# Kernel optimization log

Measured on AMD Instinct MI355X. Metric: run time of the kernel, lower is better.

Reference implementation:

```python
import jax, jax.numpy as jnp
import numpy as np

D_MODEL, D_STATE, D_CONV, EXPAND = 1024, 16, 4, 2
D_INNER = EXPAND * D_MODEL           # 2048
DT_RANK = D_MODEL // 16              # 64
BATCH, SEQLEN = 2, 2048


def setup_inputs() -> dict:
    key = jax.random.key(0)
    ks = jax.random.split(key, 10)
    s = 0.02
    hidden_states = jax.random.normal(ks[0], (BATCH, SEQLEN, D_MODEL), jnp.float32)
    in_proj_w = jax.random.normal(ks[1], (2 * D_INNER, D_MODEL), jnp.float32) * s
    conv_w = jax.random.normal(ks[2], (D_INNER, 1, D_CONV), jnp.float32) * 0.3
    conv_b = jax.random.normal(ks[3], (D_INNER,), jnp.float32) * 0.1
    x_proj_w = jax.random.normal(ks[4], (DT_RANK + 2 * D_STATE, D_INNER), jnp.float32) * s
    dt_init_std = DT_RANK ** -0.5
    dt_proj_w = jax.random.uniform(ks[5], (D_INNER, DT_RANK), jnp.float32,
                                   minval=-dt_init_std, maxval=dt_init_std)
    # bias = inverse-softplus of dt sampled log-uniform in [1e-3, 1e-1]
    dt = jnp.exp(jax.random.uniform(ks[6], (D_INNER,), jnp.float32)
                 * (np.log(0.1) - np.log(0.001)) + np.log(0.001))
    dt = jnp.clip(dt, 1e-4, None)
    dt_proj_b = dt + jnp.log(-jnp.expm1(-dt))
    # A = repeat(arange(1, d_state+1), 'n -> d n')
    A_log = jnp.log(jnp.tile(jnp.arange(1, D_STATE + 1, dtype=jnp.float32), (D_INNER, 1)))
    Dp = jnp.ones((D_INNER,), jnp.float32)
    out_proj_w = jax.random.normal(ks[7], (D_MODEL, D_INNER), jnp.float32) * s
    return {
        'hidden_states': hidden_states, 'in_proj_w': in_proj_w,
        'conv_w': conv_w, 'conv_b': conv_b, 'x_proj_w': x_proj_w,
        'dt_proj_w': dt_proj_w, 'dt_proj_b': dt_proj_b,
        'A_log': A_log, 'D': Dp, 'out_proj_w': out_proj_w,
    }


def _mamba_fwd(hidden_states, in_proj_w, conv_w, conv_b, x_proj_w,
               dt_proj_w, dt_proj_b, A_log, D, out_proj_w):
    d_inner = in_proj_w.shape[0] // 2
    d_conv = conv_w.shape[-1]
    dt_rank = dt_proj_w.shape[1]
    d_state = A_log.shape[1]
    b = hidden_states.shape[0]

    # in_proj then split into x / z gate branches  -> [B, L, d_inner] each
    xz = hidden_states @ in_proj_w.T
    x, z = jnp.split(xz, 2, axis=-1)

    # depthwise causal conv1d + SiLU (pad left d_conv-1 == padding=d_conv-1 then trim)
    xc = x.transpose(0, 2, 1)                       # [B, d_inner, L]
    xc = jax.lax.conv_general_dilated(
        xc, conv_w, window_strides=(1,), padding=[(d_conv - 1, 0)],
        dimension_numbers=('NCH', 'OIH', 'NCH'), feature_group_count=d_inner)
    xl = jax.nn.silu(xc + conv_b[None, :, None]).transpose(0, 2, 1)  # [B, L, d_inner]

    # x_proj -> dt, B, C
    x_dbl = xl @ x_proj_w.T                         # [B, L, dt_rank + 2*d_state]
    dt, Bm, Cm = jnp.split(x_dbl, [dt_rank, dt_rank + d_state], axis=-1)
    delta = jax.nn.softplus(dt @ dt_proj_w.T + dt_proj_b)  # [B, L, d_inner]

    A = -jnp.exp(A_log)                             # [d_inner, d_state]

    def step(h, inputs):
        u_t, d_t, b_t, c_t = inputs  # [B,d_inner], [B,d_inner], [B,d_state], [B,d_state]
        dA = jnp.exp(d_t[..., None] * A)                      # [B, d_inner, d_state]
        h = dA * h + (d_t * u_t)[..., None] * b_t[:, None, :]
        y_t = jnp.einsum('bdn,bn->bd', h, c_t)
        return h, y_t

    h0 = jnp.zeros((b, d_inner, d_state), hidden_states.dtype)
    xs = (xl.transpose(1, 0, 2), delta.transpose(1, 0, 2),
          Bm.transpose(1, 0, 2), Cm.transpose(1, 0, 2))
    _, ys = jax.lax.scan(step, h0, xs)              # ys: [L, B, d_inner]
    y = ys.transpose(1, 0, 2)

    y = y + xl * D                                  # skip (D) term
    y = y * jax.nn.silu(z)                          # gate
    return y @ out_proj_w.T                         # [B, L, d_model]


def reference(hidden_states, in_proj_w, conv_w, conv_b, x_proj_w,
              dt_proj_w, dt_proj_b, A_log, D, out_proj_w):
    return _mamba_fwd(hidden_states, in_proj_w, conv_w, conv_b, x_proj_w,
                      dt_proj_w, dt_proj_b, A_log, D, out_proj_w)
```

## Files before the change

kernel.cpp:

```cpp
#include <hip/hip_runtime.h>

#define D_MODEL 1024
#define D_STATE 16
#define D_CONV  4
#define D_INNER 2048
#define DT_RANK 64
#define BATCH   2
#define SEQLEN  2048
#define NTOK    (BATCH * SEQLEN)
#define NCH     64
#define LC      (SEQLEN / NCH)
#define XKS     8
#define XNC     96


__device__ __forceinline__ float bf2f(unsigned short v) {
    union { unsigned int u; float f; } c; c.u = ((unsigned int)v) << 16; return c.f;
}
__device__ __forceinline__ unsigned short f2bf(float f) {
    union { unsigned int u; float f; } c; c.f = f;
    unsigned int r = c.u + 0x7FFF + ((c.u >> 16) & 1);
    return (unsigned short)(r >> 16);
}

__device__ __forceinline__ int sniff_bf(const void* Dp) {
    return (((const unsigned int*)Dp)[0] == 0x3F803F80u) ? 1 : 0;
}

__device__ __forceinline__ float ldF(const void* p, size_t idx, int isbf) {
    return isbf ? bf2f(((const unsigned short*)p)[idx]) : ((const float*)p)[idx];
}
__device__ __forceinline__ void ld16f(const float* p, float* o) {
#pragma unroll
    for (int q = 0; q < 4; q++) {
        float4 v = *(const float4*)(p + 4 * q);
        o[4 * q + 0] = v.x; o[4 * q + 1] = v.y; o[4 * q + 2] = v.z; o[4 * q + 3] = v.w;
    }
}

#define CVT_N0 (NTOK * D_MODEL)
#define CVT_N1 (2 * D_INNER * D_MODEL)
#define CVT_N2 (D_MODEL * D_INNER)
#define CVT_N3 (D_INNER * DT_RANK)
#define CVT_TOT (CVT_N0 + CVT_N1 + CVT_N2 + CVT_N3)

__device__ __forceinline__ void cvt8(const void* in, unsigned short* out,
                                     size_t e0, int isbf)
{
    if (isbf) {
        *(uint4*)(out + e0) = *(const uint4*)((const unsigned short*)in + e0);
    } else {
        const float* f = (const float*)in + e0;
        float4 a = *(const float4*)f;
        float4 b = *(const float4*)(f + 4);
        ushort4 o0 = { f2bf(a.x), f2bf(a.y), f2bf(a.z), f2bf(a.w) };
        ushort4 o1 = { f2bf(b.x), f2bf(b.y), f2bf(b.z), f2bf(b.w) };
        *(ushort4*)(out + e0)     = o0;
        *(ushort4*)(out + e0 + 4) = o1;
    }
}

__launch_bounds__(256)
__global__ void cvt_all(const void* __restrict__ hid, const void* __restrict__ ipw,
                        const void* __restrict__ opw, const void* __restrict__ dtw,
                        unsigned short* __restrict__ hidB, unsigned short* __restrict__ ipwB,
                        unsigned short* __restrict__ opwB, unsigned short* __restrict__ dtwB,
                        const void* __restrict__ Dp)
{
    const int isbf = sniff_bf(Dp);
    size_t e = ((size_t)blockIdx.x * 256 + threadIdx.x) * 8;
    if (e < CVT_N0) { cvt8(hid, hidB, e, isbf); return; }
    e -= CVT_N0;
    if (e < CVT_N1) { cvt8(ipw, ipwB, e, isbf); return; }
    e -= CVT_N1;
    if (e < CVT_N2) { cvt8(opw, opwB, e, isbf); return; }
    e -= CVT_N2;
    if (e < CVT_N3) { cvt8(dtw, dtwB, e, isbf); }
}

typedef __attribute__((ext_vector_type(8))) __bf16 bf16x8;
typedef __attribute__((ext_vector_type(4))) float  f32x4;

__global__ void mfma_probe(int* __restrict__ dmap) {
    __shared__ alignas(16) unsigned short As[16 * 32];
    __shared__ alignas(16) unsigned short Bs[16 * 32];
    const int t = threadIdx.x;
    const int q = t >> 4, l15 = t & 15;

    for (int idx = t; idx < 512; idx += 64) {
        As[idx] = f2bf((float)(idx >> 5));
        Bs[idx] = f2bf(0.03125f);
    }
    __syncthreads();
    bf16x8 a1 = *(const bf16x8*)&As[l15 * 32 + q * 8];
    bf16x8 b1 = *(const bf16x8*)&Bs[l15 * 32 + q * 8];
    f32x4 acc1 = {0.f, 0.f, 0.f, 0.f};
    acc1 = __builtin_amdgcn_mfma_f32_16x16x32_bf16(a1, b1, acc1, 0, 0, 0);
    __syncthreads();

    for (int idx = t; idx < 512; idx += 64) {
        As[idx] = f2bf(0.03125f);
        Bs[idx] = f2bf((float)(idx >> 5));
    }
    __syncthreads();
    bf16x8 a2 = *(const bf16x8*)&As[l15 * 32 + q * 8];
    bf16x8 b2 = *(const bf16x8*)&Bs[l15 * 32 + q * 8];
    f32x4 acc2 = {0.f, 0.f, 0.f, 0.f};
    acc2 = __builtin_amdgcn_mfma_f32_16x16x32_bf16(a2, b2, acc2, 0, 0, 0);

#pragma unroll
    for (int r = 0; r < 4; r++) {
        int ma = (int)(acc1[r] + 0.5f);
        int nb = (int)(acc2[r] + 0.5f);
        if (ma < 0 || ma > 15 || nb < 0 || nb > 15) { ma = q * 4 + r; nb = l15; }
        dmap[t * 4 + r] = ma | (nb << 4);
    }
}

__device__ __forceinline__ void gl2lds16(const void* g, void* l) {
    __builtin_amdgcn_global_load_lds(
        (const __attribute__((address_space(1))) unsigned int*)g,
        (__attribute__((address_space(3))) unsigned int*)l,
        16, 0, 0);
}

__device__ __forceinline__ void stage_half(const unsigned short* __restrict__ G,
                                           int grow0, int K, int k0,
                                           unsigned short* ldsAB, int half, int t)
{
    const int r8  = t >> 3;
    const int c8  = t & 7;
    const int swz = (c8 ^ (r8 & 7)) << 3;
#pragma unroll
    for (int j = 0; j < 2; j++) {
        const int row = half * 128 + j * 64 + r8;
        gl2lds16(&G[(size_t)(grow0 + row) * K + k0 + swz],
                 &ldsAB[row * 64 + c8 * 8]);
    }
}

__device__ __forceinline__ bf16x8 ldsfrag(const unsigned short* p, int row, int slot) {
    return *(const bf16x8*)&p[row * 64 + ((slot ^ (row & 7)) << 3)];
}

__launch_bounds__(512)
__global__ void gemm1_8ph(const unsigned short* __restrict__ A,
                          const unsigned short* __restrict__ B,
                          float* __restrict__ C,
                          int M, int N, int K,
                          const int* __restrict__ dmap)
{
    extern __shared__ __align__(16) unsigned short lds[];
    unsigned short* A0l = lds;
    unsigned short* B0l = lds + 16384;
    unsigned short* A1l = lds + 32768;
    unsigned short* B1l = lds + 49152;

    const int t    = threadIdx.x;
    const int lane = t & 63;
    const int w    = t >> 6;
    const int wm   = (w >> 2) * 128, wn = (w & 3) * 64;
    const int q    = lane >> 4, l15 = lane & 15;

    const int nbn  = N >> 8;
    const int nwg  = (M >> 8) * nbn;
    const int orig = blockIdx.x;
    const int wg   = (orig & 7) * (nwg >> 3) + (orig >> 3);
    const int bm   = wg / nbn, bn = wg % nbn;
    const int m0   = bm << 8, n0 = bn << 8;
    const int NT   = K >> 6;

    int mp[4];
#pragma unroll
    for (int r = 0; r < 4; r++) mp[r] = dmap[lane * 4 + r];

    f32x4 acc[8][4];
#pragma unroll
    for (int i = 0; i < 8; i++)
#pragma unroll
        for (int j = 0; j < 4; j++) acc[i][j] = (f32x4){0.f, 0.f, 0.f, 0.f};

    stage_half(B, n0, K, 0, B0l, 0, t);
    stage_half(B, n0, K, 0, B0l, 1, t);
    stage_half(A, m0, K, 0, A0l, 0, t);
    stage_half(A, m0, K, 0, A0l, 1, t);
    {
        const int k1 = (NT > 1 ? 64 : 0);
        stage_half(B, n0, K, k1, B1l, 0, t);
        stage_half(B, n0, K, k1, B1l, 1, t);
    }
    asm volatile("s_waitcnt vmcnt(4)" ::: "memory");
    __builtin_amdgcn_s_barrier();

#pragma unroll 2
    for (int tt = 0; tt < NT; ++tt) {
        const int p = tt & 1;
        const unsigned short* Ac = p ? A1l : A0l;
        const unsigned short* Bc = p ? B1l : B0l;
        unsigned short* Anx = p ? A0l : A1l;
        unsigned short* Bnx = p ? B1l : B0l;
        const int kA = (tt + 1 < NT ? tt + 1 : 0) << 6;
        const int kB = (tt + 2 < NT ? tt + 2 : 0) << 6;

        bf16x8 af[4][2], b0r[2][2], b1r[2][2];

#pragma unroll
        for (int i = 0; i < 4; i++)
#pragma unroll
            for (int ks = 0; ks < 2; ks++)
                af[i][ks] = ldsfrag(Ac, wm + i * 16 + l15, ks * 4 + q);
#pragma unroll
        for (int j = 0; j < 2; j++)
#pragma unroll
            for (int ks = 0; ks < 2; ks++)
                b0r[j][ks] = ldsfrag(Bc, wn + j * 16 + l15, ks * 4 + q);
        stage_half(A, m0, K, kA, Anx, 0, t);
        asm volatile("" ::: "memory");
        __builtin_amdgcn_s_barrier();
        __builtin_amdgcn_s_setprio(1);
#pragma unroll
        for (int i = 0; i < 4; i++)
#pragma unroll
            for (int j = 0; j < 2; j++)
#pragma unroll
                for (int ks = 0; ks < 2; ks++)
                    acc[i][j] = __builtin_amdgcn_mfma_f32_16x16x32_bf16(
                        af[i][ks], b0r[j][ks], acc[i][j], 0, 0, 0);
        __builtin_amdgcn_s_setprio(0);
        asm volatile("" ::: "memory");
        __builtin_amdgcn_s_barrier();

#pragma unroll
        for (int j = 0; j < 2; j++)
#pragma unroll
            for (int ks = 0; ks < 2; ks++)
                b1r[j][ks] = ldsfrag(Bc, wn + 32 + j * 16 + l15, ks * 4 + q);
        stage_half(A, m0, K, kA, Anx, 1, t);
        asm volatile("" ::: "memory");
        __builtin_amdgcn_s_barrier();
        __builtin_amdgcn_s_setprio(1);
#pragma unroll
        for (int i = 0; i < 4; i++)
#pragma unroll
            for (int j = 0; j < 2; j++)
#pragma unroll
                for (int ks = 0; ks < 2; ks++)
                    acc[i][2 + j] = __builtin_amdgcn_mfma_f32_16x16x32_bf16(
                        af[i][ks], b1r[j][ks], acc[i][2 + j], 0, 0, 0);
        __builtin_amdgcn_s_setprio(0);
        asm volatile("" ::: "memory");
        __builtin_amdgcn_s_barrier();

#pragma unroll
        for (int i = 0; i < 4; i++)
#pragma unroll
            for (int ks = 0; ks < 2; ks++)
                af[i][ks] = ldsfrag(Ac, wm + 64 + i * 16 + l15, ks * 4 + q);
        stage_half(B, n0, K, kB, Bnx, 0, t);
        asm volatile("" ::: "memory");
        __builtin_amdgcn_s_barrier();
        __builtin_amdgcn_s_setprio(1);
#pragma unroll
        for (int i = 0; i < 4; i++)
#pragma unroll
            for (int j = 0; j < 2; j++)
#pragma unroll
                for (int ks = 0; ks < 2; ks++)
                    acc[4 + i][2 + j] = __builtin_amdgcn_mfma_f32_16x16x32_bf16(
                        af[i][ks], b1r[j][ks], acc[4 + i][2 + j], 0, 0, 0);
        __builtin_amdgcn_s_setprio(0);
        asm volatile("" ::: "memory");
        __builtin_amdgcn_s_barrier();

        stage_half(B, n0, K, kB, Bnx, 1, t);
        asm volatile("" ::: "memory");
        __builtin_amdgcn_s_barrier();
        __builtin_amdgcn_s_setprio(1);
#pragma unroll
        for (int i = 0; i < 4; i++)
#pragma unroll
            for (int j = 0; j < 2; j++)
#pragma unroll
                for (int ks = 0; ks < 2; ks++)
                    acc[4 + i][j] = __builtin_amdgcn_mfma_f32_16x16x32_bf16(
                        af[i][ks], b0r[j][ks], acc[4 + i][j], 0, 0, 0);
        __builtin_amdgcn_s_setprio(0);
        asm volatile("s_waitcnt vmcnt(4)" ::: "memory");
        __builtin_amdgcn_s_barrier();
    }

#pragma unroll
    for (int i = 0; i < 8; i++) {
#pragma unroll
        for (int r = 0; r < 4; r++) {
            const int mo = mp[r] & 15, no = mp[r] >> 4;
            const int m = m0 + wm + i * 16 + mo;
#pragma unroll
            for (int j = 0; j < 4; j++) {
                const int n = n0 + wn + j * 16 + no;
                C[(size_t)m * N + n] = acc[i][j][r];
            }
        }
    }
}

__device__ __forceinline__ void stage_op(const unsigned short* __restrict__ A,
                                         const unsigned short* __restrict__ B,
                                         int m0, int n0, int K, int k0,
                                         unsigned short* Al, unsigned short* Bl, int t)
{
    const int r   = t >> 3;
    const int c8  = t & 7;
    const int swz = (c8 ^ (r & 7)) << 3;
#pragma unroll
    for (int j = 0; j < 4; j++) {
        const int row = j * 32 + r;
        gl2lds16(&A[(size_t)(m0 + row) * K + k0 + swz], &Al[row * 64 + c8 * 8]);
    }
#pragma unroll
    for (int j = 0; j < 2; j++) {
        const int row = j * 32 + r;
        gl2lds16(&B[(size_t)(n0 + row) * K + k0 + swz], &Bl[row * 64 + c8 * 8]);
    }
}

__launch_bounds__(256)
__global__ void gemm_op_2ph(const unsigned short* __restrict__ A,
                            const unsigned short* __restrict__ B,
                            float* __restrict__ C,
                            const int* __restrict__ dmap)
{
    constexpr int M = NTOK, N = D_MODEL, K = D_INNER;
    constexpr int NT = K / 64;
    __shared__ alignas(16) unsigned short Al[2][128 * 64];
    __shared__ alignas(16) unsigned short Bl[2][64 * 64];

    const int t    = threadIdx.x;
    const int lane = t & 63;
    const int w    = t >> 6;
    const int wm   = (w >> 1) * 64, wn = (w & 1) * 32;
    const int q    = lane >> 4, l15 = lane & 15;

    const int nbn  = N / 64;
    const int nwg  = (M / 128) * nbn;
    const int orig = blockIdx.x;
    const int wg   = (orig & 7) * (nwg >> 3) + (orig >> 3);
    const int bm   = wg / nbn, bn = wg % nbn;
    const int m0   = bm * 128, n0 = bn * 64;

    int mp[4];
#pragma unroll
    for (int r = 0; r < 4; r++) mp[r] = dmap[lane * 4 + r];

    f32x4 acc[4][2];
#pragma unroll
    for (int i = 0; i < 4; i++)
#pragma unroll
        for (int j = 0; j < 2; j++) acc[i][j] = (f32x4){0.f, 0.f, 0.f, 0.f};

    stage_op(A, B, m0, n0, K, 0, Al[0], Bl[0], t);
    asm volatile("s_waitcnt vmcnt(0)" ::: "memory");
    __builtin_amdgcn_s_barrier();

#pragma unroll 2
    for (int tt = 0; tt < NT - 1; ++tt) {
        const int cur = tt & 1;
        stage_op(A, B, m0, n0, K, (tt + 1) * 64, Al[cur ^ 1], Bl[cur ^ 1], t);

        bf16x8 af[4][2], bfr[2][2];
#pragma unroll
        for (int i = 0; i < 4; i++)
#pragma unroll
            for (int ks = 0; ks < 2; ks++)
                af[i][ks] = ldsfrag(Al[cur], wm + i * 16 + l15, ks * 4 + q);
#pragma unroll
        for (int j = 0; j < 2; j++)
#pragma unroll
            for (int ks = 0; ks < 2; ks++)
                bfr[j][ks] = ldsfrag(Bl[cur], wn + j * 16 + l15, ks * 4 + q);
        __builtin_amdgcn_s_setprio(1);
#pragma unroll
        for (int i = 0; i < 4; i++)
#pragma unroll
            for (int j = 0; j < 2; j++)
#pragma unroll
                for (int ks = 0; ks < 2; ks++)
                    acc[i][j] = __builtin_amdgcn_mfma_f32_16x16x32_bf16(
                        af[i][ks], bfr[j][ks], acc[i][j], 0, 0, 0);
        __builtin_amdgcn_s_setprio(0);
        asm volatile("s_waitcnt vmcnt(0)" ::: "memory");
        __builtin_amdgcn_s_barrier();
    }

    {
        const int cur = (NT - 1) & 1;
        bf16x8 af[4][2], bfr[2][2];
#pragma unroll
        for (int i = 0; i < 4; i++)
#pragma unroll
            for (int ks = 0; ks < 2; ks++)
                af[i][ks] = ldsfrag(Al[cur], wm + i * 16 + l15, ks * 4 + q);
#pragma unroll
        for (int j = 0; j < 2; j++)
#pragma unroll
            for (int ks = 0; ks < 2; ks++)
                bfr[j][ks] = ldsfrag(Bl[cur], wn + j * 16 + l15, ks * 4 + q);
#pragma unroll
        for (int i = 0; i < 4; i++)
#pragma unroll
            for (int j = 0; j < 2; j++)
#pragma unroll
                for (int ks = 0; ks < 2; ks++)
                    acc[i][j] = __builtin_amdgcn_mfma_f32_16x16x32_bf16(
                        af[i][ks], bfr[j][ks], acc[i][j], 0, 0, 0);
    }

#pragma unroll
    for (int i = 0; i < 4; i++) {
#pragma unroll
        for (int r = 0; r < 4; r++) {
            const int mo = mp[r] & 15, no = mp[r] >> 4;
            const int m = m0 + wm + i * 16 + mo;
#pragma unroll
            for (int j = 0; j < 2; j++) {
                const int n = n0 + wn + j * 16 + no;
                C[(size_t)m * N + n] = acc[i][j][r];
            }
        }
    }
}

template<int EPI, int NJ, int SWAP>
__launch_bounds__(256)
__global__ void gemm_mfma_bt(const unsigned short* __restrict__ A,
                             const unsigned short* __restrict__ B,
                             float* __restrict__ C,
                             int M, int N, int K,
                             const int* __restrict__ dmap,
                             const void* __restrict__ bias,
                             const void* __restrict__ Dp)
{
    constexpr int BN = NJ * 32;
    __shared__ alignas(16) unsigned short As[128 * 32];
    __shared__ alignas(16) unsigned short Bs[BN * 32];
    const int t    = threadIdx.x;
    const int lane = t & 63;
    const int w    = t >> 6;
    const int bm   = SWAP ? blockIdx.x : blockIdx.y;
    const int bn   = SWAP ? blockIdx.y : blockIdx.x;
    const int m0   = bm * 128, n0 = bn * BN;
    const int wm   = (w >> 1) * 64, wn = (w & 1) * (NJ * 16);
    const int q    = lane >> 4, l15 = lane & 15;

    int mp[4];
#pragma unroll
    for (int r = 0; r < 4; r++) mp[r] = dmap[lane * 4 + r];

    const int srow = t >> 2;
    const int skk  = (t & 3) * 8;

    f32x4 acc[4][NJ];
#pragma unroll
    for (int i = 0; i < 4; i++)
#pragma unroll
        for (int j = 0; j < NJ; j++) acc[i][j] = (f32x4){0.f, 0.f, 0.f, 0.f};

    for (int k0 = 0; k0 < K; k0 += 32) {
        __syncthreads();
        gl2lds16(&A[(size_t)(m0 +      srow) * K + k0 + skk], &As[(     srow) * 32 + skk]);
        gl2lds16(&A[(size_t)(m0 + 64 + srow) * K + k0 + skk], &As[(64 + srow) * 32 + skk]);
#pragma unroll
        for (int jb = 0; jb < NJ / 2; jb++)
            gl2lds16(&B[(size_t)(n0 + jb * 64 + srow) * K + k0 + skk],
                     &Bs[(jb * 64 + srow) * 32 + skk]);
        __syncthreads();

        bf16x8 af[4], bfr[NJ];
#pragma unroll
        for (int i = 0; i < 4; i++)
            af[i] = *(const bf16x8*)&As[(wm + i * 16 + l15) * 32 + q * 8];
#pragma unroll
        for (int j = 0; j < NJ; j++)
            bfr[j] = *(const bf16x8*)&Bs[(wn + j * 16 + l15) * 32 + q * 8];
#pragma unroll
        for (int i = 0; i < 4; i++)
#pragma unroll
            for (int j = 0; j < NJ; j++)
                acc[i][j] = __builtin_amdgcn_mfma_f32_16x16x32_bf16(
                    af[i], bfr[j], acc[i][j], 0, 0, 0);
    }

    const int isbf = EPI ? sniff_bf(Dp) : 0;
#pragma unroll
    for (int i = 0; i < 4; i++) {
#pragma unroll
        for (int r = 0; r < 4; r++) {
            const int mo = mp[r] & 15, no = mp[r] >> 4;
            const int m = m0 + wm + i * 16 + mo;
#pragma unroll
            for (int j = 0; j < NJ; j++) {
                const int n = n0 + wn + j * 16 + no;
                float v = acc[i][j][r];
                if (EPI == 1) {
                    v += ldF(bias, n, isbf);
                    v = fmaxf(v, 0.f) + __logf(1.f + __expf(-fabsf(v)));
                }
                C[(size_t)m * N + n] = v;
            }
        }
    }
}

__launch_bounds__(256)
__global__ void xproj_splitk(const float* __restrict__ A,
                             const float* __restrict__ B,
                             float* __restrict__ part)
{
    __shared__ alignas(16) float As[16][68];
    __shared__ alignas(16) float Bs[16][68];
    const int t  = threadIdx.x;
    const int m0 = blockIdx.y * 64, n0 = blockIdx.x * 64;
    const int koff = blockIdx.z * (D_INNER / XKS);
    const int lr = t >> 2;
    const int lk = (t & 3) * 4;
    const int tm = t >> 4, tn = t & 15;

    float acc[4][4];
#pragma unroll
    for (int i = 0; i < 4; i++)
#pragma unroll
        for (int j = 0; j < 4; j++) acc[i][j] = 0.f;

    for (int k0 = koff; k0 < koff + D_INNER / XKS; k0 += 16) {
        float av[4], bv[4];
        {
            const int m = m0 + lr;
            float4 p = *(const float4*)&A[(size_t)m * D_INNER + k0 + lk];
            av[0] = p.x; av[1] = p.y; av[2] = p.z; av[3] = p.w;
        }
        {
            const int n = n0 + lr;
            if (n < XNC) {
                float4 p = *(const float4*)&B[(size_t)n * D_INNER + k0 + lk];
                bv[0] = p.x; bv[1] = p.y; bv[2] = p.z; bv[3] = p.w;
            } else { bv[0] = bv[1] = bv[2] = bv[3] = 0.f; }
        }
        __syncthreads();
#pragma unroll
        for (int i = 0; i < 4; i++) { As[lk + i][lr] = av[i]; Bs[lk + i][lr] = bv[i]; }
        __syncthreads();

#pragma unroll
        for (int kk = 0; kk < 16; kk++) {
            float4 a = *(const float4*)&As[kk][tm * 4];
            float4 b = *(const float4*)&Bs[kk][tn * 4];
            float aa[4] = { a.x, a.y, a.z, a.w };
            float bb[4] = { b.x, b.y, b.z, b.w };
#pragma unroll
            for (int i = 0; i < 4; i++)
#pragma unroll
                for (int j = 0; j < 4; j++) acc[i][j] = fmaf(aa[i], bb[j], acc[i][j]);
        }
    }

    float* out = part + (size_t)blockIdx.z * NTOK * XNC;
#pragma unroll
    for (int i = 0; i < 4; i++) {
        const int m = m0 + tm * 4 + i;
#pragma unroll
        for (int j = 0; j < 4; j++) {
            const int n = n0 + tn * 4 + j;
            if (n < XNC) out[(size_t)m * XNC + n] = acc[i][j];
        }
    }
}

__launch_bounds__(256)
__global__ void xproj_reduce(const float* __restrict__ part, float* __restrict__ xdbl,
                             unsigned short* __restrict__ xdt)
{
    const int idx = blockIdx.x * 256 + threadIdx.x;
    float s = 0.f;
#pragma unroll
    for (int z = 0; z < XKS; z++) s += part[(size_t)z * NTOK * XNC + idx];
    xdbl[idx] = s;
    const int m = idx / XNC;
    const int col = idx - m * XNC;
    if (col < 64) xdt[m * 64 + col] = f2bf(s);
}

__launch_bounds__(256)
__global__ void conv_silu(const float* __restrict__ xz,
                          const void* __restrict__ conv_w,
                          const void* __restrict__ conv_b,
                          float* __restrict__ xl,
                          const void* __restrict__ Dp)
{
    const int isbf = sniff_bf(Dp);
    const int gid = blockIdx.x * 256 + threadIdx.x;
    const int dq  = gid & (D_INNER / 4 - 1);
    const int tg  = gid >> 9;
    const int d0  = dq * 4;
    const int tok0 = tg * 4;
    const int l0  = tok0 & (SEQLEN - 1);

    float w[4][4], bias[4];
#pragma unroll
    for (int dd = 0; dd < 4; dd++) {
        bias[dd] = ldF(conv_b, d0 + dd, isbf);
#pragma unroll
        for (int j = 0; j < 4; j++) w[dd][j] = ldF(conv_w, (d0 + dd) * 4 + j, isbf);
    }

    float4 x[7];
    const float* rowp = xz + (size_t)tok0 * (2 * D_INNER) + d0;
#pragma unroll
    for (int k = 0; k < 7; k++) {
        const int off = k - 3;
        if (l0 + off >= 0)
            x[k] = *(const float4*)(rowp + (ptrdiff_t)off * (2 * D_INNER));
        else
            x[k] = (float4){0.f, 0.f, 0.f, 0.f};
    }

#pragma unroll
    for (int tn = 0; tn < 4; tn++) {
        float a0 = bias[0], a1 = bias[1], a2 = bias[2], a3 = bias[3];
#pragma unroll
        for (int j = 0; j < 4; j++) {
            const float4 v = x[tn + j];
            a0 = fmaf(v.x, w[0][j], a0);
            a1 = fmaf(v.y, w[1][j], a1);
            a2 = fmaf(v.z, w[2][j], a2);
            a3 = fmaf(v.w, w[3][j], a3);
        }
        float4 o;
        o.x = a0 / (1.f + __expf(-a0));
        o.y = a1 / (1.f + __expf(-a1));
        o.z = a2 / (1.f + __expf(-a2));
        o.w = a3 / (1.f + __expf(-a3));
        *(float4*)&xl[(size_t)(tok0 + tn) * D_INNER + d0] = o;
    }
}

__device__ __forceinline__ void mk_dA(float dv, const float An[16], int pw, float* dA)
{
    if (pw) {
        const float E = __expf(dv * An[0]);
        dA[0] = E;
        const float E2 = E * E;          dA[1] = E2;
        const float E4 = E2 * E2;        dA[3] = E4;
        const float E8 = E4 * E4;        dA[7] = E8;
        dA[2]  = E2 * E;
        dA[4]  = E4 * E;   dA[5]  = E4 * E2;  dA[6]  = dA[5] * E;
        dA[8]  = E8 * E;   dA[9]  = E8 * E2;  dA[10] = dA[9] * E;
        dA[11] = E8 * E4;  dA[12] = dA[11] * E;
        dA[13] = dA[11] * E2; dA[14] = dA[13] * E; dA[15] = E8 * E8;
    } else {
#pragma unroll
        for (int n = 0; n < 16; n++) dA[n] = __expf(dv * An[n]);
    }
}

__device__ __forceinline__ int chk_pw(const float An[16])
{
    int pw = 1;
#pragma unroll
    for (int n = 1; n < 16; n++)
        pw = pw && (fabsf(An[n] - (float)(n + 1) * An[0]) <= 3e-4f * (float)(n + 1));
    return pw;
}

__device__ __forceinline__ void scan_step(float h[16], float dv, float uv,
                                          const float Bv[16], const float An[16], int pw)
{
    float dA[16]; mk_dA(dv, An, pw, dA);
    const float du = dv * uv;
#pragma unroll
    for (int n = 0; n < 16; n++) h[n] = fmaf(dA[n], h[n], du * Bv[n]);
}

__device__ __forceinline__ float scan_step_y(float h[16], float dv, float uv,
                                             const float Bv[16], const float Cv[16],
                                             const float An[16], int pw, float Dd)
{
    float dA[16]; mk_dA(dv, An, pw, dA);
    const float du = dv * uv;
    float s[16];
#pragma unroll
    for (int n = 0; n < 16; n++) {
        h[n] = fmaf(dA[n], h[n], du * Bv[n]);
        s[n] = h[n] * Cv[n];
    }
#pragma unroll
    for (int n = 0; n < 8; n++) s[n] += s[n + 8];
#pragma unroll
    for (int n = 0; n < 4; n++) s[n] += s[n + 4];
    s[0] += s[2]; s[1] += s[3];
    return s[0] + s[1] + uv * Dd;
}

__launch_bounds__(256)
__global__ void scan_chunk(const float* __restrict__ dlt,
                           const float* __restrict__ xl,
                           const float* __restrict__ xdbl,
                           const void* __restrict__ A_log,
                           float* __restrict__ S,
                           float* __restrict__ sumD,
                           const void* __restrict__ Dp)
{
    const int isbf = sniff_bf(Dp);
    const int t  = threadIdx.x;
    const int dg = blockIdx.x & 7;
    const int c  = (blockIdx.x >> 3) & (NCH - 1);
    const int b  = blockIdx.x >> 9;
    const int d  = dg * 256 + t;

    float An[16], h[16];
#pragma unroll
    for (int n = 0; n < 16; n++) {
        An[n] = -expf(ldF(A_log, d * 16 + n, isbf));
        h[n] = 0.f;
    }
    const int pw = chk_pw(An);
    float sd = 0.f;
    const size_t r0 = (size_t)b * SEQLEN + c * LC;

    float dv0 = dlt[r0 * D_INNER + d];
    float uv0 = xl [r0 * D_INNER + d];
    float Bv0[16]; ld16f(&xdbl[r0 * 96 + 64], Bv0);

    for (int i = 0; i < LC; i += 2) {
        const size_t r1 = r0 + i + 1;
        float dv1 = dlt[r1 * D_INNER + d];
        float uv1 = xl [r1 * D_INNER + d];
        float Bv1[16]; ld16f(&xdbl[r1 * 96 + 64], Bv1);

        scan_step(h, dv0, uv0, Bv0, An, pw);
        sd += dv0;

        const size_t r2 = r0 + ((i + 2 < LC) ? (i + 2) : (i + 1));
        dv0 = dlt[r2 * D_INNER + d];
        uv0 = xl [r2 * D_INNER + d];
        ld16f(&xdbl[r2 * 96 + 64], Bv0);

        scan_step(h, dv1, uv1, Bv1, An, pw);
        sd += dv1;
    }

    const size_t base = (((size_t)b * NCH + c) * 16) * D_INNER + d;
#pragma unroll
    for (int n = 0; n < 16; n++) S[base + (size_t)n * D_INNER] = h[n];
    sumD[((size_t)b * NCH + c) * D_INNER + d] = sd;
}

__launch_bounds__(256)
__global__ void scan_combine(float* __restrict__ S,
                             const float* __restrict__ sumD,
                             const void* __restrict__ A_log,
                             const void* __restrict__ Dp)
{
    const int isbf = sniff_bf(Dp);
    const int g = blockIdx.x * 256 + threadIdx.x;
    const int d = g & (D_INNER - 1);
    const int n = (g >> 11) & 15;
    const int b = g >> 15;
    const float An = -expf(ldF(A_log, d * 16 + n, isbf));

    float hs = 0.f;
    float Sc = S[(((size_t)b * NCH + 0) * 16 + n) * D_INNER + d];
    float sd = sumD[((size_t)b * NCH + 0) * D_INNER + d];
    for (int c = 0; c < NCH; c++) {
        const int cn = (c + 1 < NCH) ? c + 1 : c;
        const float Scn = S[(((size_t)b * NCH + cn) * 16 + n) * D_INNER + d];
        const float sdn = sumD[((size_t)b * NCH + cn) * D_INNER + d];
        S[(((size_t)b * NCH + c) * 16 + n) * D_INNER + d] = hs;
        hs = fmaf(__expf(An * sd), hs, Sc);
        Sc = Scn; sd = sdn;
    }
}

__launch_bounds__(256)
__global__ void scan_apply(const float* __restrict__ dlt,
                           const float* __restrict__ xl,
                           const float* __restrict__ xdbl,
                           const float* __restrict__ xz,
                           const void* __restrict__ A_log,
                           const void* __restrict__ Dp,
                           const float* __restrict__ S,
                           unsigned short* __restrict__ yg)
{
    const int isbf = sniff_bf(Dp);
    const int t  = threadIdx.x;
    const int dg = blockIdx.x & 7;
    const int c  = (blockIdx.x >> 3) & (NCH - 1);
    const int b  = blockIdx.x >> 9;
    const int d  = dg * 256 + t;

    float An[16], h[16];
    const size_t base = (((size_t)b * NCH + c) * 16) * D_INNER + d;
#pragma unroll
    for (int n = 0; n < 16; n++) {
        An[n] = -expf(ldF(A_log, d * 16 + n, isbf));
        h[n] = S[base + (size_t)n * D_INNER];
    }
    const int pw = chk_pw(An);
    const float Dd = ldF(Dp, d, isbf);
    const size_t r0 = (size_t)b * SEQLEN + c * LC;

    float dv0 = dlt[r0 * D_INNER + d];
    float uv0 = xl [r0 * D_INNER + d];
    float zv0 = xz [r0 * (2 * D_INNER) + D_INNER + d];
    float Bv0[16], Cv0[16];
    ld16f(&xdbl[r0 * 96 + 64], Bv0);
    ld16f(&xdbl[r0 * 96 + 80], Cv0);

    for (int i = 0; i < LC; i += 2) {
        const size_t ra = r0 + i + 1;
        float dv1 = dlt[ra * D_INNER + d];
        float uv1 = xl [ra * D_INNER + d];
        float zv1 = xz [ra * (2 * D_INNER) + D_INNER + d];
        float Bv1[16], Cv1[16];
        ld16f(&xdbl[ra * 96 + 64], Bv1);
        ld16f(&xdbl[ra * 96 + 80], Cv1);

        {
            const float yv = scan_step_y(h, dv0, uv0, Bv0, Cv0, An, pw, Dd);
            yg[(r0 + i) * D_INNER + d] = f2bf(yv * (zv0 / (1.f + expf(-zv0))));
        }

        const size_t rb = r0 + ((i + 2 < LC) ? (i + 2) : (i + 1));
        dv0 = dlt[rb * D_INNER + d];
        uv0 = xl [rb * D_INNER + d];
        zv0 = xz [rb * (2 * D_INNER) + D_INNER + d];
        ld16f(&xdbl[rb * 96 + 64], Bv0);
        ld16f(&xdbl[rb * 96 + 80], Cv0);

        {
            const float yv = scan_step_y(h, dv1, uv1, Bv1, Cv1, An, pw, Dd);
            yg[ra * D_INNER + d] = f2bf(yv * (zv1 / (1.f + expf(-zv1))));
        }
    }
}

extern "C" void kernel_launch(void* const* d_in, const int* in_sizes, int n_in,
                              void* d_out, int out_size, void* d_ws, size_t ws_size,
                              hipStream_t stream)
{
    const void* hidden     = d_in[0];
    const void* in_proj_w  = d_in[1];
    const void* conv_w     = d_in[2];
    const void* conv_b     = d_in[3];
    const void* x_proj_w   = d_in[4];
    const void* dt_proj_w  = d_in[5];
    const void* dt_proj_b  = d_in[6];
    const void* A_log      = d_in[7];
    const void* Dp         = d_in[8];
    const void* out_proj_w = d_in[9];

    char* ws = (char*)d_ws;
    float*          xz   = (float*)(ws);
    float*          xl   = (float*)(ws + 67108864ull);
    float*          xdbl = (float*)(ws + 100663296ull);
    float*          dlt  = (float*)(ws + 102236160ull);
    unsigned short* yg   = (unsigned short*)(ws + 135790592ull);
    unsigned short* opwB = (unsigned short*)(ws + 152567808ull);
    unsigned short* xdt  = (unsigned short*)(ws + 156762112ull);
    unsigned short* dtwB = (unsigned short*)(ws + 157286400ull);
    float*          S    = (float*)(ws + 169345280ull);
    float*          sumD = (float*)(ws + 186122496ull);
    int*            dmap = (int*)  (ws + 187171072ull);
    unsigned short* hidB  = (unsigned short*)(ws + 102236160ull);
    unsigned short* ipwB  = (unsigned short*)(ws + 102236160ull + 8388608ull);
    float*          xpart = (float*)(ws + 102236160ull);

    dim3 blk(256);

    mfma_probe<<<dim3(1), dim3(64), 0, stream>>>(dmap);

    cvt_all<<<dim3(CVT_TOT / (256 * 8)), blk, 0, stream>>>(
        hidden, in_proj_w, out_proj_w, dt_proj_w, hidB, ipwB, opwB, dtwB, Dp);

    hipFuncSetAttribute((const void*)gemm1_8ph,
                        hipFuncAttributeMaxDynamicSharedMemorySize, 131072);
    gemm1_8ph<<<dim3((NTOK / 256) * (2 * D_INNER / 256)), dim3(512), 131072, stream>>>(
        hidB, ipwB, xz, NTOK, 2 * D_INNER, D_MODEL, dmap);

    conv_silu<<<dim3((NTOK / 4) * (D_INNER / 4) / 256), blk, 0, stream>>>(
        xz, conv_w, conv_b, xl, Dp);

    xproj_splitk<<<dim3(2, 64, XKS), blk, 0, stream>>>(
        xl, (const float*)x_proj_w, xpart);
    xproj_reduce<<<dim3(NTOK * XNC / 256), blk, 0, stream>>>(xpart, xdbl, xdt);

    gemm_mfma_bt<1, 4, 0><<<dim3(16, 32), blk, 0, stream>>>(
        xdt, dtwB, dlt, NTOK, D_INNER, DT_RANK, dmap, dt_proj_b, Dp);

    scan_chunk<<<dim3(BATCH * NCH * (D_INNER / 256)), blk, 0, stream>>>(
        dlt, xl, xdbl, A_log, S, sumD, Dp);
    scan_combine<<<dim3(BATCH * 16 * D_INNER / 256), blk, 0, stream>>>(
        S, sumD, A_log, Dp);
    scan_apply<<<dim3(BATCH * NCH * (D_INNER / 256)), blk, 0, stream>>>(
        dlt, xl, xdbl, xz, A_log, Dp, S, yg);

    gemm_op_2ph<<<dim3((NTOK / 128) * (D_MODEL / 64)), blk, 0, stream>>>(
        yg, opwB, (float*)d_out, dmap);
}
```

Before: 317.5 us.

## Fuse causal depthwise conv1d and SiLU into in_proj GEMM epilogue

The in_proj GEMM now applies the causal conv and SiLU itself for x-branch tiles and writes xl directly. The separate conv_silu kernel and its fp32 round trip of the x half of xz are removed. To obtain the three preceding rows, each x tile stages an extra 16-row halo of A and computes it with extra MFMAs in one wave group, then stages tile outputs through LDS. This adds redundant halo compute, extra LDS use and extra barriers inside the GEMM, and the epilogue is serialized over two passes.

```diff
diff --git a/kernel.cpp b/kernel.cpp
--- a/kernel.cpp
+++ b/kernel.cpp
@@ -144,17 +144,24 @@
 }
 
 __launch_bounds__(512)
-__global__ void gemm1_8ph(const unsigned short* __restrict__ A,
-                          const unsigned short* __restrict__ B,
-                          float* __restrict__ C,
-                          int M, int N, int K,
-                          const int* __restrict__ dmap)
-{
+__global__ void gemm1_conv(const unsigned short* __restrict__ A,
+                           const unsigned short* __restrict__ B,
+                           float* __restrict__ xzC,
+                           float* __restrict__ xl,
+                           const void* __restrict__ conv_w,
+                           const void* __restrict__ conv_b,
+                           const void* __restrict__ Dp,
+                           const int* __restrict__ dmap)
+{
+    constexpr int M = NTOK, N = 2 * D_INNER, K = D_MODEL;
+    constexpr int NT = K >> 6;
     extern __shared__ __align__(16) unsigned short lds[];
     unsigned short* A0l = lds;
     unsigned short* B0l = lds + 16384;
     unsigned short* A1l = lds + 32768;
     unsigned short* B1l = lds + 49152;
+    __shared__ alignas(16) unsigned short haloA[2][16 * 64];
+    __shared__ alignas(16) float xhalo[3][256];
 
     const int t    = threadIdx.x;
     const int lane = t & 63;
@@ -168,7 +175,7 @@
     const int wg   = (orig & 7) * (nwg >> 3) + (orig >> 3);
     const int bm   = wg / nbn, bn = wg % nbn;
     const int m0   = bm << 8, n0 = bn << 8;
-    const int NT   = K >> 6;
+    const int isx  = (bn < 8);
 
     int mp[4];
 #pragma unroll
@@ -179,11 +186,24 @@
     for (int i = 0; i < 8; i++)
 #pragma unroll
         for (int j = 0; j < 4; j++) acc[i][j] = (f32x4){0.f, 0.f, 0.f, 0.f};
+    f32x4 acch[4];
+#pragma unroll
+    for (int j = 0; j < 4; j++) acch[j] = (f32x4){0.f, 0.f, 0.f, 0.f};
+
+    auto stage_halo = [&](int k0, unsigned short* Hbuf) {
+        if (isx && t < 128) {
+            const int r8 = t >> 3, c8 = t & 7;
+            const int swz = (c8 ^ (r8 & 7)) << 3;
+            int grow = m0 - 16 + r8; if (grow < 0) grow = 0;
+            gl2lds16(&A[(size_t)grow * K + k0 + swz], &Hbuf[r8 * 64 + c8 * 8]);
+        }
+    };
 
     stage_half(B, n0, K, 0, B0l, 0, t);
     stage_half(B, n0, K, 0, B0l, 1, t);
     stage_half(A, m0, K, 0, A0l, 0, t);
     stage_half(A, m0, K, 0, A0l, 1, t);
+    stage_halo(0, haloA[0]);
     {
         const int k1 = (NT > 1 ? 64 : 0);
         stage_half(B, n0, K, k1, B1l, 0, t);
@@ -197,12 +217,14 @@
         const int p = tt & 1;
         const unsigned short* Ac = p ? A1l : A0l;
         const unsigned short* Bc = p ? B1l : B0l;
+        const unsigned short* Hc = haloA[p];
         unsigned short* Anx = p ? A0l : A1l;
         unsigned short* Bnx = p ? B1l : B0l;
+        unsigned short* Hnx = haloA[p ^ 1];
         const int kA = (tt + 1 < NT ? tt + 1 : 0) << 6;
         const int kB = (tt + 2 < NT ? tt + 2 : 0) << 6;
 
-        bf16x8 af[4][2], b0r[2][2], b1r[2][2];
+        bf16x8 af[4][2], b0r[2][2], b1r[2][2], afh[2];
 
 #pragma unroll
         for (int i = 0; i < 4; i++)
@@ -214,6 +236,10 @@
 #pragma unroll
             for (int ks = 0; ks < 2; ks++)
                 b0r[j][ks] = ldsfrag(Bc, wn + j * 16 + l15, ks * 4 + q);
+        if (isx && (w >> 2) == 0)
+#pragma unroll
+            for (int ks = 0; ks < 2; ks++)
+                afh[ks] = ldsfrag(Hc, l15, ks * 4 + q);
         stage_half(A, m0, K, kA, Anx, 0, t);
         asm volatile("" ::: "memory");
         __builtin_amdgcn_s_barrier();
@@ -226,6 +252,13 @@
                 for (int ks = 0; ks < 2; ks++)
                     acc[i][j] = __builtin_amdgcn_mfma_f32_16x16x32_bf16(
                         af[i][ks], b0r[j][ks], acc[i][j], 0, 0, 0);
+        if (isx && (w >> 2) == 0)
+#pragma unroll
+            for (int j = 0; j < 2; j++)
+#pragma unroll
+                for (int ks = 0; ks < 2; ks++)
+                    acch[j] = __builtin_amdgcn_mfma_f32_16x16x32_bf16(
+                        afh[ks], b0r[j][ks], acch[j], 0, 0, 0);
         __builtin_amdgcn_s_setprio(0);
         asm volatile("" ::: "memory");
         __builtin_amdgcn_s_barrier();
@@ -236,6 +269,7 @@
             for (int ks = 0; ks < 2; ks++)
                 b1r[j][ks] = ldsfrag(Bc, wn + 32 + j * 16 + l15, ks * 4 + q);
         stage_half(A, m0, K, kA, Anx, 1, t);
+        stage_halo(kA, Hnx);
         asm volatile("" ::: "memory");
         __builtin_amdgcn_s_barrier();
         __builtin_amdgcn_s_setprio(1);
@@ -247,6 +281,13 @@
                 for (int ks = 0; ks < 2; ks++)
                     acc[i][2 + j] = __builtin_amdgcn_mfma_f32_16x16x32_bf16(
                         af[i][ks], b1r[j][ks], acc[i][2 + j], 0, 0, 0);
+        if (isx && (w >> 2) == 0)
+#pragma unroll
+            for (int j = 0; j < 2; j++)
+#pragma unroll
+                for (int ks = 0; ks < 2; ks++)
+                    acch[2 + j] = __builtin_amdgcn_mfma_f32_16x16x32_bf16(
+                        afh[ks], b1r[j][ks], acch[2 + j], 0, 0, 0);
         __builtin_amdgcn_s_setprio(0);
         asm volatile("" ::: "memory");
         __builtin_amdgcn_s_barrier();
@@ -289,18 +330,109 @@
         __builtin_amdgcn_s_barrier();
     }
 
-#pragma unroll
-    for (int i = 0; i < 8; i++) {
-#pragma unroll
-        for (int r = 0; r < 4; r++) {
-            const int mo = mp[r] & 15, no = mp[r] >> 4;
-            const int m = m0 + wm + i * 16 + mo;
-#pragma unroll
-            for (int j = 0; j < 4; j++) {
-                const int n = n0 + wn + j * 16 + no;
-                C[(size_t)m * N + n] = acc[i][j][r];
+    asm volatile("s_waitcnt vmcnt(0)" ::: "memory");
+    __syncthreads();
+
+    if (!isx) {
+#pragma unroll
+        for (int i = 0; i < 8; i++) {
+#pragma unroll
+            for (int r = 0; r < 4; r++) {
+                const int mo = mp[r] & 15, no = mp[r] >> 4;
+                const int m = m0 + wm + i * 16 + mo;
+#pragma unroll
+                for (int j = 0; j < 4; j++) {
+                    const int n = n0 + wn + j * 16 + no;
+                    xzC[(size_t)m * N + n] = acc[i][j][r];
+                }
             }
         }
+        return;
+    }
+
+    float* xs = (float*)lds;
+    const int isbf = sniff_bf(Dp);
+    const int cq = t & 63, c0 = cq * 4, tokg = t >> 6;
+    float wv[4][4], bvv[4];
+#pragma unroll
+    for (int dd = 0; dd < 4; dd++) {
+        bvv[dd] = ldF(conv_b, n0 + c0 + dd, isbf);
+#pragma unroll
+        for (int kk = 0; kk < 4; kk++)
+            wv[dd][kk] = ldF(conv_w, (size_t)(n0 + c0 + dd) * 4 + kk, isbf);
+    }
+
+#pragma unroll
+    for (int pass = 0; pass < 2; ++pass) {
+        const int tb = pass * 128;
+        if ((w >> 2) == pass) {
+#pragma unroll
+            for (int i = 0; i < 8; i++)
+#pragma unroll
+                for (int r = 0; r < 4; r++) {
+                    const int mo = mp[r] & 15, no = mp[r] >> 4;
+#pragma unroll
+                    for (int j = 0; j < 4; j++)
+                        xs[(i * 16 + mo) * 256 + wn + j * 16 + no] = acc[i][j][r];
+                }
+        }
+        if ((w >> 2) == 0) {
+            if (pass == 0) {
+#pragma unroll
+                for (int r = 0; r < 4; r++) {
+                    const int mo = mp[r] & 15, no = mp[r] >> 4;
+                    if (mo >= 13)
+#pragma unroll
+                        for (int j = 0; j < 4; j++)
+                            xhalo[mo - 13][wn + j * 16 + no] = acch[j][r];
+                }
+            } else {
+#pragma unroll
+                for (int r = 0; r < 4; r++) {
+                    const int mo = mp[r] & 15, no = mp[r] >> 4;
+                    if (mo >= 13)
+#pragma unroll
+                        for (int j = 0; j < 4; j++)
+                            xhalo[mo - 13][wn + j * 16 + no] = acc[7][j][r];
+                }
+            }
+        }
+        __syncthreads();
+
+        const int tk0 = tokg * 16;
+        float4 win[3];
+#pragma unroll
+        for (int k = 0; k < 3; k++) {
+            const int ri = tk0 - 3 + k;
+            win[k] = (ri < 0) ? *(const float4*)&xhalo[ri + 3][c0]
+                              : *(const float4*)&xs[ri * 256 + c0];
+        }
+#pragma unroll
+        for (int tk16 = 0; tk16 < 16; ++tk16) {
+            const int tk = tk0 + tk16;
+            const float4 cur = *(const float4*)&xs[tk * 256 + c0];
+            const int g = m0 + tb + tk;
+            const int lpos = g & (SEQLEN - 1);
+            float a0 = bvv[0], a1 = bvv[1], a2 = bvv[2], a3 = bvv[3];
+#pragma unroll
+            for (int kk = 0; kk < 4; kk++) {
+                if (lpos - 3 + kk >= 0) {
+                    const float4 v = (kk == 3) ? cur : win[kk];
+                    a0 = fmaf(v.x, wv[0][kk], a0);
+                    a1 = fmaf(v.y, wv[1][kk], a1);
+                    a2 = fmaf(v.z, wv[2][kk], a2);
+                    a3 = fmaf(v.w, wv[3][kk], a3);
+                }
+            }
+            float4 o;
+            o.x = a0 / (1.f + __expf(-a0));
+            o.y = a1 / (1.f + __expf(-a1));
+            o.z = a2 / (1.f + __expf(-a2));
+            o.w = a3 / (1.f + __expf(-a3));
+            *(float4*)&xl[(size_t)g * D_INNER + n0 + c0] = o;
+            win[0] = win[1]; win[1] = win[2]; win[2] = cur;
+        }
+        __syncthreads();
     }
 }
 
@@ -587,60 +719,6 @@
     const int m = idx / XNC;
     const int col = idx - m * XNC;
     if (col < 64) xdt[m * 64 + col] = f2bf(s);
-}
-
-__launch_bounds__(256)
-__global__ void conv_silu(const float* __restrict__ xz,
-                          const void* __restrict__ conv_w,
-                          const void* __restrict__ conv_b,
-                          float* __restrict__ xl,
-                          const void* __restrict__ Dp)
-{
-    const int isbf = sniff_bf(Dp);
-    const int gid = blockIdx.x * 256 + threadIdx.x;
-    const int dq  = gid & (D_INNER / 4 - 1);
-    const int tg  = gid >> 9;
-    const int d0  = dq * 4;
-    const int tok0 = tg * 4;
-    const int l0  = tok0 & (SEQLEN - 1);
-
-    float w[4][4], bias[4];
-#pragma unroll
-    for (int dd = 0; dd < 4; dd++) {
-        bias[dd] = ldF(conv_b, d0 + dd, isbf);
-#pragma unroll
-        for (int j = 0; j < 4; j++) w[dd][j] = ldF(conv_w, (d0 + dd) * 4 + j, isbf);
-    }
-
-    float4 x[7];
-    const float* rowp = xz + (size_t)tok0 * (2 * D_INNER) + d0;
-#pragma unroll
-    for (int k = 0; k < 7; k++) {
-        const int off = k - 3;
-        if (l0 + off >= 0)
-            x[k] = *(const float4*)(rowp + (ptrdiff_t)off * (2 * D_INNER));
-        else
-            x[k] = (float4){0.f, 0.f, 0.f, 0.f};
-    }
-
-#pragma unroll
-    for (int tn = 0; tn < 4; tn++) {
-        float a0 = bias[0], a1 = bias[1], a2 = bias[2], a3 = bias[3];
-#pragma unroll
-        for (int j = 0; j < 4; j++) {
-            const float4 v = x[tn + j];
-            a0 = fmaf(v.x, w[0][j], a0);
-            a1 = fmaf(v.y, w[1][j], a1);
-            a2 = fmaf(v.z, w[2][j], a2);
-            a3 = fmaf(v.w, w[3][j], a3);
-        }
-        float4 o;
-        o.x = a0 / (1.f + __expf(-a0));
-        o.y = a1 / (1.f + __expf(-a1));
-        o.z = a2 / (1.f + __expf(-a2));
-        o.w = a3 / (1.f + __expf(-a3));
-        *(float4*)&xl[(size_t)(tok0 + tn) * D_INNER + d0] = o;
-    }
 }
 
 __device__ __forceinline__ void mk_dA(float dv, const float An[16], int pw, float* dA)
@@ -881,13 +959,10 @@
     cvt_all<<<dim3(CVT_TOT / (256 * 8)), blk, 0, stream>>>(
         hidden, in_proj_w, out_proj_w, dt_proj_w, hidB, ipwB, opwB, dtwB, Dp);
 
-    hipFuncSetAttribute((const void*)gemm1_8ph,
+    hipFuncSetAttribute((const void*)gemm1_conv,
                         hipFuncAttributeMaxDynamicSharedMemorySize, 131072);
-    gemm1_8ph<<<dim3((NTOK / 256) * (2 * D_INNER / 256)), dim3(512), 131072, stream>>>(
-        hidB, ipwB, xz, NTOK, 2 * D_INNER, D_MODEL, dmap);
-
-    conv_silu<<<dim3((NTOK / 4) * (D_INNER / 4) / 256), blk, 0, stream>>>(
-        xz, conv_w, conv_b, xl, Dp);
+    gemm1_conv<<<dim3((NTOK / 256) * (2 * D_INNER / 256)), dim3(512), 131072, stream>>>(
+        hidB, ipwB, xz, xl, conv_w, conv_b, Dp, dmap);
 
     xproj_splitk<<<dim3(2, 64, XKS), blk, 0, stream>>>(
         xl, (const float*)x_proj_w, xpart);
```

Result: slower. 347.6 us (+9.5%).
